# Kernel optimization log

Measured on AMD Instinct MI355X. Metric: run time of the kernel, lower is better.

## Reference

```python
import math
import jax, jax.numpy as jnp
import numpy as np

D_MODEL = 1024
N_HEAD = 16
HEAD_DIM = D_MODEL // N_HEAD
B, T = 2, 2048


def _layernorm(x, g, b, eps=1e-5):
    mu = jnp.mean(x, axis=-1, keepdims=True)
    var = jnp.mean(jnp.square(x - mu), axis=-1, keepdims=True)
    return (x - mu) * jax.lax.rsqrt(var + eps) * g + b


def _l2norm(x, eps=1e-12):
    n = jnp.sqrt(jnp.sum(jnp.square(x), axis=-1, keepdims=True))
    return x / jnp.maximum(n, eps)


def _rope(x, times):
    # x: [B,T,H,Dh] (Dh even), times: [T]
    half = x.shape[-1] // 2
    freqs = jnp.exp(-jnp.arange(half, dtype=x.dtype) * (math.log(10000.0) / half))
    theta = times[:, None] * freqs[None, :]              # [T, half]
    cos = jnp.cos(theta)[None, :, None, :]               # [1,T,1,half]
    sin = jnp.sin(theta)[None, :, None, :]
    xr = x.reshape(*x.shape[:-1], half, 2)
    x1, x2 = xr[..., 0], xr[..., 1]
    r1 = x1 * cos - x2 * sin
    r2 = x1 * sin + x2 * cos
    return jnp.stack([r1, r2], axis=-1).reshape(x.shape)


def setup_inputs() -> dict:
    key = jax.random.key(0)
    ks = jax.random.split(key, 16)
    s = 0.02
    f32 = jnp.float32
    inp = {
        'x': jax.random.normal(ks[0], (B, T, D_MODEL), f32),
        'Wq': jax.random.normal(ks[1], (D_MODEL, D_MODEL), f32) * s,
        'Wk': jax.random.normal(ks[2], (D_MODEL, D_MODEL), f32) * s,
        'Wv': jax.random.normal(ks[3], (D_MODEL, D_MODEL), f32) * s,
        'gate_w': jax.random.normal(ks[4], (D_MODEL, D_MODEL), f32) * s,
        'gate_b': jnp.zeros((D_MODEL,), f32),
        'p_w': jax.random.normal(ks[5], (D_MODEL, D_MODEL), f32) * s,
        'p_b': jnp.zeros((D_MODEL,), f32),
        'out_w': jax.random.normal(ks[6], (D_MODEL, D_MODEL), f32) * s,
        'out_b': jnp.zeros((D_MODEL,), f32),
        'clock_w': jax.random.normal(ks[7], (D_MODEL, N_HEAD), f32) * s,
        'clock_b': jnp.zeros((N_HEAD,), f32),
        'ln1_g': jnp.ones((D_MODEL,), f32), 'ln1_b': jnp.zeros((D_MODEL,), f32),
        'ln2_g': jnp.ones((D_MODEL,), f32), 'ln2_b': jnp.zeros((D_MODEL,), f32),
        'mlp_w1': jax.random.normal(ks[8], (D_MODEL, 4 * D_MODEL), f32) * s,
        'mlp_b1': jnp.zeros((4 * D_MODEL,), f32),
        'mlp_w2': jax.random.normal(ks[9], (4 * D_MODEL, D_MODEL), f32) * s,
        'mlp_b2': jnp.zeros((D_MODEL,), f32),
    }
    return inp


def reference(x, Wq, Wk, Wv, gate_w, gate_b, p_w, p_b, out_w, out_b,
              clock_w, clock_b, ln1_g, ln1_b, ln2_g, ln2_b,
              mlp_w1, mlp_b1, mlp_w2, mlp_b2):
    Bx, Tx, D = x.shape
    H, Dh = N_HEAD, HEAD_DIM
    residual = x
    xn = _layernorm(x, ln1_g, ln1_b)
    times = jnp.arange(Tx, dtype=x.dtype)

    q = _l2norm((xn @ Wq).reshape(Bx, Tx, H, Dh))
    k = _l2norm((xn @ Wk).reshape(Bx, Tx, H, Dh))
    v = (xn @ Wv).reshape(Bx, Tx, H, Dh)
    clock = jax.nn.softplus(xn @ clock_w + clock_b).reshape(Bx, Tx, H, 1)

    q = _rope(q, times)
    k = _rope(k, times)

    gj = -jax.nn.softplus(xn @ gate_w + gate_b).reshape(Bx, Tx, H, Dh)
    gcp = jnp.exp(jnp.clip(jnp.cumsum(gj, axis=1), -60.0, 50.0))
    q = q * gcp
    k = k / (gcp + 1e-8)

    p = (xn @ p_w + p_b).reshape(Bx, Tx, H, Dh)
    p_max = jnp.max(p, axis=1, keepdims=True)
    p_exp = jnp.exp(p - p_max) * clock
    p_cs = jnp.cumsum(p_exp, axis=1)
    q = q / (p_cs + 1e-8)
    k = k * p_exp

    # causal softmax attention (SDPA, scale = 1/sqrt(Dh))
    scores = jnp.einsum('bqhd,bkhd->bhqk', q, k) / math.sqrt(Dh)
    mask = jnp.tril(jnp.ones((Tx, Tx), dtype=bool))
    scores = jnp.where(mask[None, None], scores, -jnp.inf)
    attn = jax.nn.softmax(scores, axis=-1)
    out = jnp.einsum('bhqk,bkhd->bqhd', attn, v).reshape(Bx, Tx, D)

    out = out @ out_w + out_b
    x1 = out + residual
    h = _layernorm(x1, ln2_g, ln2_b)
    h = jax.nn.gelu(h @ mlp_w1 + mlp_b1, approximate=False) @ mlp_w2 + mlp_b2
    return x1 + h
```

## Files before the change

kernel.cpp:

```cpp
#include <hip/hip_runtime.h>
#include <hip/hip_bf16.h>
#include <math.h>

typedef __hip_bfloat16 bf16;
typedef __attribute__((ext_vector_type(8))) short short8;
typedef __attribute__((ext_vector_type(4))) short short4v;
typedef __attribute__((ext_vector_type(4))) float f32x4;

#define BT   4096
#define DM   1024
#define NH   16
#define DH   64
#define TSEQ 2048

__device__ __forceinline__ float wave_sum(float v){
#pragma unroll
  for (int o = 32; o; o >>= 1) v += __shfl_xor(v, o);
  return v;
}

__device__ __forceinline__ float block_sum(float v){
  __shared__ float sm[4];
  v = wave_sum(v);
  __syncthreads();
  if ((threadIdx.x & 63) == 0) sm[threadIdx.x >> 6] = v;
  __syncthreads();
  return sm[0] + sm[1] + sm[2] + sm[3];
}

__device__ __forceinline__ float softplusf(float x){
  return x > 20.f ? x : __logf(1.f + __expf(x));
}

__device__ __forceinline__ short f2bf(float f){
  unsigned u = __builtin_bit_cast(unsigned, f);
  u += 0x7FFF + ((u >> 16) & 1);
  return (short)(u >> 16);
}

__device__ __forceinline__ short8 ld8(const short* p){
  short4v a = *(const short4v*)p;
  short4v b = *(const short4v*)(p + 4);
  short8 r;
  r[0]=a[0]; r[1]=a[1]; r[2]=a[2]; r[3]=a[3];
  r[4]=b[0]; r[5]=b[1]; r[6]=b[2]; r[7]=b[3];
  return r;
}

__device__ __forceinline__ void async16(const short* g, short* l){
  __builtin_amdgcn_global_load_lds(
      (const __attribute__((address_space(1))) void*)g,
      (__attribute__((address_space(3))) void*)l, 16, 0, 0);
}

__device__ __forceinline__ int xcd_swizzle(int lin, int nwg){
  const int q = nwg >> 3, r = nwg & 7;
  const int xcd = lin & 7, i = lin >> 3;
  return (xcd < r ? xcd * (q + 1) : r * (q + 1) + (xcd - r) * q) + i;
}

__device__ __forceinline__ void wt_body(const float* __restrict__ src,
    short* __restrict__ dst, int K, int N){
  __shared__ short T[32][33];
  const int tx = threadIdx.x & 31, ty = threadIdx.x >> 5;
  const int n0 = blockIdx.x << 5, k0 = blockIdx.y << 5;
#pragma unroll
  for (int r = 0; r < 4; r++){
    const int k = k0 + (ty << 2) + r;
    const int n = n0 + tx;
    T[tx][(ty << 2) + r] = (n < N) ? f2bf(src[(long)k * N + n]) : (short)0;
  }
  __syncthreads();
#pragma unroll
  for (int r = 0; r < 4; r++){
    const int n = n0 + (ty << 2) + r;
    if (n < N) dst[(long)n * K + k0 + tx] = T[(ty << 2) + r][tx];
  }
}

__global__ __launch_bounds__(256) void wt_kernel(const float* __restrict__ src,
    short* __restrict__ dst, int K, int N){
  wt_body(src, dst, K, N);
}

__global__ __launch_bounds__(256) void wt6_kernel(
    const float* s0, const float* s1, const float* s2, const float* s3,
    const float* s4, const float* s5,
    short* d0, short* d1, short* d2, short* d3, short* d4, short* d5){
  const float* src; short* dst;
  switch (blockIdx.z){
    case 0: src = s0; dst = d0; break;
    case 1: src = s1; dst = d1; break;
    case 2: src = s2; dst = d2; break;
    case 3: src = s3; dst = d3; break;
    case 4: src = s4; dst = d4; break;
    default: src = s5; dst = d5; break;
  }
  wt_body(src, dst, DM, DM);
}

__global__ __launch_bounds__(256) void biascat_fill(const float* __restrict__ gb,
    const float* __restrict__ pb, const float* __restrict__ cb, float* __restrict__ out){
  const int i = blockIdx.x * 256 + threadIdx.x;
  if (i >= 5136) return;
  float v = 0.f;
  if (i >= 5120) v = cb[i - 5120];
  else if (i >= 4096) v = pb[i - 4096];
  else if (i >= 3072) v = gb[i - 3072];
  out[i] = v;
}

__global__ __launch_bounds__(256) void ln_kernel(const float* __restrict__ xin,
    const float* __restrict__ g, const float* __restrict__ bb, short* __restrict__ out){
  const long row = blockIdx.x;
  const int tid = threadIdx.x;
  float v[4];
#pragma unroll
  for (int i = 0; i < 4; i++) v[i] = xin[row * DM + tid + i * 256];
  float s = block_sum(v[0] + v[1] + v[2] + v[3]);
  const float mu = s * (1.f / DM);
  float d2 = 0.f;
#pragma unroll
  for (int i = 0; i < 4; i++){ float dd = v[i] - mu; d2 = fmaf(dd, dd, d2); }
  d2 = block_sum(d2);
  const float rstd = rsqrtf(d2 * (1.f / DM) + 1e-5f);
#pragma unroll
  for (int i = 0; i < 4; i++){
    int c = tid + i * 256;
    out[row * DM + c] = f2bf(fmaf((v[i] - mu) * rstd, g[c], bb[c]));
  }
}

template <int EPI>
__global__ __launch_bounds__(256) void gemm_bt(
    const short* __restrict__ A, const short* __restrict__ Bt,
    const float* __restrict__ bias, const float* __restrict__ resf,
    const float* __restrict__ bias2, float* __restrict__ Cf2,
    float* __restrict__ Cf, short* __restrict__ Cbf, int M, int N, int K)
{
  __shared__ __attribute__((aligned(16))) short As[3][4096];
  __shared__ __attribute__((aligned(16))) short Bs[3][4096];
  const int tid = threadIdx.x;
  const int lane = tid & 63, w = tid >> 6;
  const int l16 = lane & 15, quad = lane >> 4;
  const int wm = w >> 1, wn = w & 1;
  const int gx = (int)gridDim.x, gy = (int)gridDim.y;
  int wg = xcd_swizzle((int)blockIdx.x + gx * ((int)blockIdx.y + gy * (int)blockIdx.z),
                       gx * gy * (int)gridDim.z);
  const int bx = wg % gx; wg /= gx;
  const int by = wg % gy; wg /= gy;
  const int bz = wg;
  const int bm0 = by << 7, bn0 = bx << 7;
  const int ks = K / (int)gridDim.z;
  const int kbeg = bz * ks;
  const int nt = ks >> 5;

  const int csw = (tid >> 3) & 3;
  const int r0 = tid >> 2,        c0 = (tid & 3) ^ csw;
  const int r1 = 64 + (tid >> 2);
  const short* ga0 = A  + (long)(bm0 + r0) * K + kbeg + c0 * 8;
  const short* ga1 = A  + (long)(bm0 + r1) * K + kbeg + c0 * 8;
  const short* gb0 = Bt + (long)min(bn0 + r0, N - 1) * K + kbeg + c0 * 8;
  const short* gb1 = Bt + (long)min(bn0 + r1, N - 1) * K + kbeg + c0 * 8;
  const int wofs = w << 9;

#define STAGE(buf, t) do {                                   \
    const long ko_ = (long)(t) * 32;                         \
    async16(ga0 + ko_, &As[buf][wofs]);                      \
    async16(gb0 + ko_, &Bs[buf][wofs]);                      \
    async16(ga1 + ko_, &As[buf][2048 + wofs]);               \
    async16(gb1 + ko_, &Bs[buf][2048 + wofs]);               \
  } while (0)

  f32x4 acc[4][4] = {};

  STAGE(0, 0);
  if (nt > 1) STAGE(1, 1);

  const int qsw = (quad ^ ((l16 >> 1) & 3)) * 8;

  int cur = 0, stg = 2;
  for (int t = 0; t < nt; t++){
    if (t + 1 < nt){
      asm volatile("s_waitcnt vmcnt(4)" ::: "memory");
    } else {
      asm volatile("s_waitcnt vmcnt(0)" ::: "memory");
    }
    __builtin_amdgcn_s_barrier();
    __builtin_amdgcn_sched_barrier(0);
    if (t + 2 < nt) STAGE(stg, t + 2);
    short8 af[4], bfr[4];
#pragma unroll
    for (int i = 0; i < 4; i++){
      af[i]  = *(const short8*)&As[cur][(wm * 64 + i * 16 + l16) * 32 + qsw];
      bfr[i] = *(const short8*)&Bs[cur][(wn * 64 + i * 16 + l16) * 32 + qsw];
    }
#pragma unroll
    for (int i = 0; i < 4; i++)
#pragma unroll
      for (int j = 0; j < 4; j++)
        acc[i][j] = __builtin_amdgcn_mfma_f32_16x16x32_bf16(af[i], bfr[j], acc[i][j], 0, 0, 0);
    cur = (cur == 2) ? 0 : cur + 1;
    stg = (stg == 2) ? 0 : stg + 1;
  }
#undef STAGE

#pragma unroll
  for (int i = 0; i < 4; i++){
#pragma unroll
    for (int r = 0; r < 4; r++){
      const int row = bm0 + wm * 64 + i * 16 + quad * 4 + r;
#pragma unroll
      for (int j = 0; j < 4; j++){
        const int col = bn0 + wn * 64 + j * 16 + l16;
        if (col < N){
          float v = acc[i][j][r];
          const long off = (long)row * N + col;
          if constexpr (EPI >= 1 && EPI != 6) v += bias[col];
          if constexpr (EPI == 2 || EPI == 4) v += resf[off];
          if constexpr (EPI == 3){
            v = 0.5f * v * (1.f + erff(v * 0.70710678118654752f));
            Cbf[off] = f2bf(v);
          } else if constexpr (EPI == 4){
            Cf[off] = v;
            Cf2[off] = v + bias2[col];
          } else if constexpr (EPI == 6){
            unsafeAtomicAdd(&Cf[off], v);
          } else {
            Cf[off] = v;
          }
        }
      }
    }
  }
}

template <int EPI>
__global__ __launch_bounds__(256, 2) void gemm_bt2(
    const short* __restrict__ A, const short* __restrict__ Bt,
    const float* __restrict__ bias, const float* __restrict__ resf,
    float* __restrict__ Cf, short* __restrict__ Cbf, int M, int N, int K)
{
  __shared__ __attribute__((aligned(16))) short As[3][8192];
  __shared__ __attribute__((aligned(16))) short Bs[3][4096];
  const int tid = threadIdx.x;
  const int lane = tid & 63, w = tid >> 6;
  const int l16 = lane & 15, quad = lane >> 4;
  const int wm = w >> 1, wn = w & 1;
  const int gx = (int)gridDim.x, gy = (int)gridDim.y;
  int wg = xcd_swizzle((int)blockIdx.x + gx * ((int)blockIdx.y + gy * (int)blockIdx.z),
                       gx * gy * (int)gridDim.z);
  const int bx = wg % gx; wg /= gx;
  const int by = wg % gy; wg /= gy;
  const int bz = wg;
  const int bm0 = by << 8, bn0 = bx << 7;
  const int ks = K / (int)gridDim.z;
  const int kbeg = bz * ks;
  const int nt = ks >> 5;

  const int csw = (tid >> 3) & 3;
  const int c0 = (tid & 3) ^ csw;
  const int ra = tid >> 2;
  const short* ga0 = A  + (long)(bm0 + ra)       * K + kbeg + c0 * 8;
  const short* ga1 = A  + (long)(bm0 + 64 + ra)  * K + kbeg + c0 * 8;
  const short* ga2 = A  + (long)(bm0 + 128 + ra) * K + kbeg + c0 * 8;
  const short* ga3 = A  + (long)(bm0 + 192 + ra) * K + kbeg + c0 * 8;
  const short* gb0 = Bt + (long)min(bn0 + ra, N - 1)      * K + kbeg + c0 * 8;
  const short* gb1 = Bt + (long)min(bn0 + 64 + ra, N - 1) * K + kbeg + c0 * 8;
  const int wofs = w << 9;

#define STAGE2(buf, t) do {                                  \
    const long ko_ = (long)(t) * 32;                         \
    async16(ga0 + ko_, &As[buf][wofs]);                      \
    async16(ga1 + ko_, &As[buf][2048 + wofs]);               \
    async16(ga2 + ko_, &As[buf][4096 + wofs]);               \
    async16(ga3 + ko_, &As[buf][6144 + wofs]);               \
    async16(gb0 + ko_, &Bs[buf][wofs]);                      \
    async16(gb1 + ko_, &Bs[buf][2048 + wofs]);               \
  } while (0)

  f32x4 acc[8][4] = {};

  STAGE2(0, 0);
  if (nt > 1) STAGE2(1, 1);

  const int qsw = (quad ^ ((l16 >> 1) & 3)) * 8;

  int cur = 0, stg = 2;
  for (int t = 0; t < nt; t++){
    if (t + 1 < nt){
      asm volatile("s_waitcnt vmcnt(6)" ::: "memory");
    } else {
      asm volatile("s_waitcnt vmcnt(0)" ::: "memory");
    }
    __builtin_amdgcn_s_barrier();
    __builtin_amdgcn_sched_barrier(0);
    if (t + 2 < nt) STAGE2(stg, t + 2);
    short8 af[8], bfr[4];
#pragma unroll
    for (int i = 0; i < 8; i++)
      af[i]  = *(const short8*)&As[cur][(wm * 128 + i * 16 + l16) * 32 + qsw];
#pragma unroll
    for (int j = 0; j < 4; j++)
      bfr[j] = *(const short8*)&Bs[cur][(wn * 64 + j * 16 + l16) * 32 + qsw];
#pragma unroll
    for (int i = 0; i < 8; i++)
#pragma unroll
      for (int j = 0; j < 4; j++)
        acc[i][j] = __builtin_amdgcn_mfma_f32_16x16x32_bf16(af[i], bfr[j], acc[i][j], 0, 0, 0);
    cur = (cur == 2) ? 0 : cur + 1;
    stg = (stg == 2) ? 0 : stg + 1;
  }
#undef STAGE2

#pragma unroll
  for (int i = 0; i < 8; i++){
#pragma unroll
    for (int r = 0; r < 4; r++){
      const int row = bm0 + wm * 128 + i * 16 + quad * 4 + r;
#pragma unroll
      for (int j = 0; j < 4; j++){
        const int col = bn0 + wn * 64 + j * 16 + l16;
        if (col < N){
          float v = acc[i][j][r];
          const long off = (long)row * N + col;
          if constexpr (EPI >= 1 && EPI != 6) v += bias[col];
          if constexpr (EPI == 2) v += resf[off];
          if constexpr (EPI == 3){
            v = 0.5f * v * (1.f + erff(v * 0.70710678118654752f));
            Cbf[off] = f2bf(v);
          } else if constexpr (EPI == 5){
            if (col < 5120)
              Cf[(long)(col >> 10) * 4194304 + (long)row * 1024 + (col & 1023)] = v;
            else
              Cf[20971520 + (long)row * 16 + (col - 5120)] = v;
          } else if constexpr (EPI == 6){
            unsafeAtomicAdd(&Cf[off], v);
          } else {
            Cf[off] = v;
          }
        }
      }
    }
  }
}

__global__ __launch_bounds__(256) void scan_p1(float* __restrict__ G, const float* __restrict__ P,
    const float* __restrict__ Vf, short* __restrict__ Vh,
    float* __restrict__ cmax, float* __restrict__ gsum){
  const int tid = blockIdx.x * 256 + threadIdx.x;
  const int d = tid & 63, c = (tid >> 6) & 31, bh = tid >> 11;
  const int h = bh & 15, b = bh >> 4;
  const long base = (((long)(b * TSEQ + c * 64)) * NH + h) * 64 + d;
  float mx = -1e30f, gs = 0.f;
  for (int tt = 0; tt < 64; tt++){
    const long idx = base + (long)tt * (NH * 64);
    float gj = -softplusf(G[idx]);
    G[idx] = gj;
    gs += gj;
    mx = fmaxf(mx, P[idx]);
    Vh[idx] = f2bf(Vf[idx]);
  }
  const int chain = bh * 64 + d;
  cmax[chain * 32 + c] = mx;
  gsum[chain * 32 + c] = gs;
}

__global__ void scan_p2(const float* __restrict__ cmax, const float* __restrict__ gsum,
                        float* __restrict__ pmax, float* __restrict__ gpre){
  const int chain = blockIdx.x * 256 + threadIdx.x;
  float mx = -1e30f;
  for (int c = 0; c < 32; c++) mx = fmaxf(mx, cmax[chain * 32 + c]);
  pmax[chain] = mx;
  float run = 0.f;
  for (int c = 0; c < 32; c++){ gpre[chain * 32 + c] = run; run += gsum[chain * 32 + c]; }
}

__global__ __launch_bounds__(256) void scan_p3(const float* __restrict__ G, float* __restrict__ P,
    const float* __restrict__ CLKr, float* __restrict__ Q, float* __restrict__ K,
    const float* __restrict__ pmax, const float* __restrict__ gpre, float* __restrict__ psum){
  const int tid = blockIdx.x * 256 + threadIdx.x;
  const int d = tid & 63, c = (tid >> 6) & 31, bh = tid >> 11;
  const int h = bh & 15, b = bh >> 4;
  const int chain = bh * 64 + d;
  const long base = (((long)(b * TSEQ + c * 64)) * NH + h) * 64 + d;
  const float pm = pmax[chain];
  const float freq = expf(-(float)(d >> 1) * 0.28782313662425575f);
  float sn = sinf((float)(c * 64) * freq);
  float cn = cosf((float)(c * 64) * freq);
  const float sf = sinf(freq), cf = cosf(freq);
  float grun = gpre[chain * 32 + c];
  float ps = 0.f;
  for (int tt = 0; tt < 64; tt++){
    const long idx = base + (long)tt * (NH * 64);
    const int t = c * 64 + tt;
    float clk = softplusf(CLKr[(long)(b * TSEQ + t) * NH + h]);
    float pe = __expf(P[idx] - pm) * clk;
    P[idx] = pe; ps += pe;
    grun += G[idx];
    float gc = __expf(fminf(fmaxf(grun, -60.f), 50.f));
    {
      float q = Q[idx];
      float n = sqrtf(wave_sum(q * q));
      q = q / fmaxf(n, 1e-12f);
      float pr = __shfl_xor(q, 1);
      q = (d & 1) ? fmaf(pr, sn, q * cn) : fmaf(q, cn, -pr * sn);
      Q[idx] = q * gc;
    }
    {
      float k = K[idx];
      float n = sqrtf(wave_sum(k * k));
      k = k / fmaxf(n, 1e-12f);
      float pr = __shfl_xor(k, 1);
      k = (d & 1) ? fmaf(pr, sn, k * cn) : fmaf(k, cn, -pr * sn);
      K[idx] = k / (gc + 1e-8f);
    }
    const float ns = fmaf(sn, cf, cn * sf);
    const float nc = fmaf(cn, cf, -sn * sf);
    sn = ns; cn = nc;
  }
  psum[chain * 32 + c] = ps;
}

__global__ void scan_p4(const float* __restrict__ psum, float* __restrict__ ppre){
  const int chain = blockIdx.x * 256 + threadIdx.x;
  float run = 0.f;
  for (int c = 0; c < 32; c++){ ppre[chain * 32 + c] = run; run += psum[chain * 32 + c]; }
}

__global__ __launch_bounds__(256) void scan_p5(const float* __restrict__ P, const float* __restrict__ Q,
    const float* __restrict__ K, const float* __restrict__ ppre,
    short* __restrict__ Qh, short* __restrict__ Kh){
  const int tid = blockIdx.x * 256 + threadIdx.x;
  const int d = tid & 63, c = (tid >> 6) & 31, bh = tid >> 11;
  const int h = bh & 15, b = bh >> 4;
  const int chain = bh * 64 + d;
  const long base = (((long)(b * TSEQ + c * 64)) * NH + h) * 64 + d;
  float cs = ppre[chain * 32 + c];
  for (int tt = 0; tt < 64; tt++){
    const long idx = base + (long)tt * (NH * 64);
    float pe = P[idx];
    cs += pe;
    Qh[idx] = f2bf(Q[idx] / (cs + 1e-8f) * 0.125f);
    Kh[idx] = f2bf(K[idx] * pe);
  }
}

__global__ __launch_bounds__(256) void fattn_kernel(const short* __restrict__ Qh,
    const short* __restrict__ Kh, const short* __restrict__ Vh, short* __restrict__ O){
  __shared__ __attribute__((aligned(16))) short Ks[64][72];
  __shared__ __attribute__((aligned(16))) short Vt[64][68];
  __shared__ __attribute__((aligned(16))) short Ps[4][16][72];
  const int tid  = threadIdx.x;
  const int lane = tid & 63, w = tid >> 6;
  const int quad = lane >> 4, l16 = lane & 15;
  const int gx = (int)gridDim.x;
  int wgs = xcd_swizzle((int)blockIdx.x + gx * (int)blockIdx.y, gx * (int)gridDim.y);
  const int bxs = wgs % gx;
  const int bh = wgs / gx, h = bh & 15, b = bh >> 4;
  const int qt = gx - 1 - bxs;
  const int q0  = qt << 6;
  const int qw0 = q0 + w * 16;
  const long strideT = NH * DH;
  const long base_bh = ((long)b * TSEQ * NH + h) * DH;

  const short* qp = Qh + base_bh + (long)(qw0 + l16) * strideT + quad * 8;
  const short8 qa0 = *(const short8*)qp;
  const short8 qa1 = *(const short8*)(qp + 32);

  f32x4 oacc[4] = {{0,0,0,0},{0,0,0,0},{0,0,0,0},{0,0,0,0}};
  float lpart[4] = {0.f,0.f,0.f,0.f};

  const int krow = tid >> 2, kcol = (tid & 3) << 4;
  const int vkey = tid & 63, vd0 = (tid >> 6) << 4;
  const short* kbase = Kh + base_bh + (long)krow * strideT + kcol;
  const short* vbase = Vh + base_bh + (long)vkey * strideT + vd0;

  short8 kr0 = *(const short8*)kbase;
  short8 kr1 = *(const short8*)(kbase + 8);
  short8 vr0 = *(const short8*)vbase;
  short8 vr1 = *(const short8*)(vbase + 8);

  const int ntiles = qt + 1;
  for (int t = 0; t < ntiles; t++){
    *(short8*)&Ks[krow][kcol]     = kr0;
    *(short8*)&Ks[krow][kcol + 8] = kr1;
#pragma unroll
    for (int j = 0; j < 8; j++) Vt[vd0 + j][vkey] = vr0[j];
#pragma unroll
    for (int j = 0; j < 8; j++) Vt[vd0 + 8 + j][vkey] = vr1[j];
    __syncthreads();
    if (t + 1 < ntiles){
      const long off = (long)(t + 1) * (64 * strideT);
      kr0 = *(const short8*)(kbase + off);
      kr1 = *(const short8*)(kbase + off + 8);
      vr0 = *(const short8*)(vbase + off);
      vr1 = *(const short8*)(vbase + off + 8);
    }
    const int kt0 = t << 6;
    f32x4 c[4] = {{0,0,0,0},{0,0,0,0},{0,0,0,0},{0,0,0,0}};
#pragma unroll
    for (int kg = 0; kg < 4; kg++){
      const short8 b0 = ld8(&Ks[kg * 16 + l16][quad * 8]);
      const short8 b1 = ld8(&Ks[kg * 16 + l16][32 + quad * 8]);
      c[kg] = __builtin_amdgcn_mfma_f32_16x16x32_bf16(qa0, b0, c[kg], 0, 0, 0);
      c[kg] = __builtin_amdgcn_mfma_f32_16x16x32_bf16(qa1, b1, c[kg], 0, 0, 0);
    }
    if (kt0 + 63 > qw0){
#pragma unroll
      for (int kg = 0; kg < 4; kg++)
#pragma unroll
        for (int r = 0; r < 4; r++){
          const int qq = qw0 + quad * 4 + r;
          if (kt0 + kg * 16 + l16 > qq) c[kg][r] = -1e30f;
        }
    }
#pragma unroll
    for (int kg = 0; kg < 4; kg++)
#pragma unroll
      for (int r = 0; r < 4; r++) c[kg][r] = __expf(c[kg][r] - 0.25f);
#pragma unroll
    for (int r = 0; r < 4; r++)
      lpart[r] += (c[0][r] + c[1][r]) + (c[2][r] + c[3][r]);
#pragma unroll
    for (int kg = 0; kg < 4; kg++)
#pragma unroll
      for (int r = 0; r < 4; r++)
        Ps[w][quad * 4 + r][kg * 16 + l16] = f2bf(c[kg][r]);
    const short8 pa0 = ld8(&Ps[w][l16][quad * 8]);
    const short8 pa1 = ld8(&Ps[w][l16][32 + quad * 8]);
#pragma unroll
    for (int f = 0; f < 4; f++){
      const short8 vb0 = ld8(&Vt[f * 16 + l16][quad * 8]);
      const short8 vb1 = ld8(&Vt[f * 16 + l16][32 + quad * 8]);
      oacc[f] = __builtin_amdgcn_mfma_f32_16x16x32_bf16(pa0, vb0, oacc[f], 0, 0, 0);
      oacc[f] = __builtin_amdgcn_mfma_f32_16x16x32_bf16(pa1, vb1, oacc[f], 0, 0, 0);
    }
    __syncthreads();
  }
#pragma unroll
  for (int r = 0; r < 4; r++){
    float l = lpart[r];
#pragma unroll
    for (int o = 1; o <= 8; o <<= 1) l += __shfl_xor(l, o);
    const float inv = 1.f / l;
    const long row = base_bh + (long)(qw0 + quad * 4 + r) * strideT + l16;
#pragma unroll
    for (int f = 0; f < 4; f++) O[row + f * 16] = f2bf(oacc[f][r] * inv);
  }
}

extern "C" void kernel_launch(void* const* d_in, const int* in_sizes, int n_in,
                              void* d_out, int out_size, void* d_ws, size_t ws_size,
                              hipStream_t stream){
  const float* x       = (const float*)d_in[0];
  const float* Wq      = (const float*)d_in[1];
  const float* Wk      = (const float*)d_in[2];
  const float* Wv      = (const float*)d_in[3];
  const float* gate_w  = (const float*)d_in[4];
  const float* gate_b  = (const float*)d_in[5];
  const float* p_w     = (const float*)d_in[6];
  const float* p_b     = (const float*)d_in[7];
  const float* out_w   = (const float*)d_in[8];
  const float* out_b   = (const float*)d_in[9];
  const float* clock_w = (const float*)d_in[10];
  const float* clock_b = (const float*)d_in[11];
  const float* ln1_g   = (const float*)d_in[12];
  const float* ln1_b   = (const float*)d_in[13];
  const float* ln2_g   = (const float*)d_in[14];
  const float* ln2_b   = (const float*)d_in[15];
  const float* mlp_w1  = (const float*)d_in[16];
  const float* mlp_b1  = (const float*)d_in[17];
  const float* mlp_w2  = (const float*)d_in[18];
  const float* mlp_b2  = (const float*)d_in[19];
  float* outp = (float*)d_out;

  float* ws   = (float*)d_ws;
  float* C5   = ws;
  float* Qb   = ws;
  float* Kb   = ws + 4194304;
  float* Vf   = ws + 8388608;
  float* Gb   = ws + 12582912;
  float* Pb   = ws + 16777216;
  float* CLKr = ws + 20971520;
  float* cmax = CLKr + 65536;
  float* gsum = cmax + 65536;
  float* gpre = gsum + 65536;
  float* pmax = gpre + 65536;
  float* biascat = cmax;
  short* sb   = (short*)(ws + 21235712);
  short* XNb  = sb;
  short* Vh   = sb;
  short* WcT  = sb + 4194304;
  short* OwT  = WcT + 5260288;
  short* W1T  = OwT + 1048576;
  short* W2T  = W1T + 4194304;
  short* Qh  = (short*)(ws + 8388608);
  short* Kh  = (short*)(ws + 8388608 + 2097152);
  short* MID = (short*)ws;
  short* Ob  = (short*)(ws + 12582912);
  short* Hb  = (short*)(ws + 12582912 + 2097152);
  float* X1  = Pb;

  wt6_kernel<<<dim3(32, 32, 6), 256, 0, stream>>>(
      Wq, Wk, Wv, gate_w, p_w, out_w,
      WcT, WcT + 1048576, WcT + 2097152, WcT + 3145728, WcT + 4194304, OwT);
  wt_kernel<<<dim3(1, 32), 256, 0, stream>>>(clock_w, WcT + 5242880, DM, NH);
  wt_kernel<<<dim3(128, 32), 256, 0, stream>>>(mlp_w1, W1T, DM, 4 * DM);
  wt_kernel<<<dim3(32, 128), 256, 0, stream>>>(mlp_w2, W2T, 4 * DM, DM);
  biascat_fill<<<21, 256, 0, stream>>>(gate_b, p_b, clock_b, biascat);

  ln_kernel<<<BT, 256, 0, stream>>>(x, ln1_g, ln1_b, XNb);

  gemm_bt2<5><<<dim3(41, BT / 256), 256, 0, stream>>>(
      XNb, WcT, biascat, nullptr, C5, nullptr, BT, 5136, DM);

  scan_p1<<<256, 256, 0, stream>>>(Gb, Pb, Vf, Vh, cmax, gsum);
  scan_p2<<<8, 256, 0, stream>>>(cmax, gsum, pmax, gpre);
  scan_p3<<<256, 256, 0, stream>>>(Gb, Pb, CLKr, Qb, Kb, pmax, gpre, gsum);
  scan_p4<<<8, 256, 0, stream>>>(gsum, gpre);
  scan_p5<<<256, 256, 0, stream>>>(Pb, Qb, Kb, gpre, Qh, Kh);

  fattn_kernel<<<dim3(TSEQ / 64, 2 * NH), 256, 0, stream>>>(Qh, Kh, Vh, Ob);

  gemm_bt<4><<<dim3(DM / 128, BT / 128), 256, 0, stream>>>(
      Ob, OwT, out_b, x, mlp_b2, outp, X1, nullptr, BT, DM, DM);
  ln_kernel<<<BT, 256, 0, stream>>>(X1, ln2_g, ln2_b, Hb);
  gemm_bt2<3><<<dim3(4 * DM / 128, BT / 256), 256, 0, stream>>>(
      Hb, W1T, mlp_b1, nullptr, nullptr, MID, BT, 4 * DM, DM);
  gemm_bt2<6><<<dim3(DM / 128, BT / 256, 4), 256, 0, stream>>>(
      MID, W2T, nullptr, nullptr, outp, nullptr, BT, DM, 4 * DM);
}
```

Measured before the change: 644.1 us.

## Enlarge GEMM tiles to 256x256 with 512 threads and K=64 double buffering

Replaces the 256x128 triple-buffered GEMM (256 threads, K-step 32) with a 256x256 tile version using 8 waves, a K-step of 64, double buffering and an 8-way XOR swizzle. It also raises wave priority around the MFMA blocks. The aim is more operand reuse per LDS load and fewer barriers per FLOP for the big projection and MLP GEMMs. In exchange the grid has fewer blocks (for example 21x16 for the fused projection and 64 for the split-K down-projection), which risks occupancy and tail effects, and it uses 128KB of LDS per block.

```diff
diff --git a/kernel.cpp b/kernel.cpp
--- a/kernel.cpp
+++ b/kernel.cpp
@@ -236,82 +236,86 @@
 }
 
 template <int EPI>
-__global__ __launch_bounds__(256, 2) void gemm_bt2(
+__global__ __launch_bounds__(512, 2) void gemm_bt3(
     const short* __restrict__ A, const short* __restrict__ Bt,
-    const float* __restrict__ bias, const float* __restrict__ resf,
+    const float* __restrict__ bias,
     float* __restrict__ Cf, short* __restrict__ Cbf, int M, int N, int K)
 {
-  __shared__ __attribute__((aligned(16))) short As[3][8192];
-  __shared__ __attribute__((aligned(16))) short Bs[3][4096];
+  __shared__ __attribute__((aligned(16))) short As[2][16384];
+  __shared__ __attribute__((aligned(16))) short Bs[2][16384];
   const int tid = threadIdx.x;
   const int lane = tid & 63, w = tid >> 6;
   const int l16 = lane & 15, quad = lane >> 4;
-  const int wm = w >> 1, wn = w & 1;
+  const int wm = w >> 2, wn = w & 3;
   const int gx = (int)gridDim.x, gy = (int)gridDim.y;
   int wg = xcd_swizzle((int)blockIdx.x + gx * ((int)blockIdx.y + gy * (int)blockIdx.z),
                        gx * gy * (int)gridDim.z);
   const int bx = wg % gx; wg /= gx;
   const int by = wg % gy; wg /= gy;
   const int bz = wg;
-  const int bm0 = by << 8, bn0 = bx << 7;
+  const int bm0 = by << 8, bn0 = bx << 8;
   const int ks = K / (int)gridDim.z;
   const int kbeg = bz * ks;
-  const int nt = ks >> 5;
-
-  const int csw = (tid >> 3) & 3;
-  const int c0 = (tid & 3) ^ csw;
-  const int ra = tid >> 2;
-  const short* ga0 = A  + (long)(bm0 + ra)       * K + kbeg + c0 * 8;
-  const short* ga1 = A  + (long)(bm0 + 64 + ra)  * K + kbeg + c0 * 8;
-  const short* ga2 = A  + (long)(bm0 + 128 + ra) * K + kbeg + c0 * 8;
-  const short* ga3 = A  + (long)(bm0 + 192 + ra) * K + kbeg + c0 * 8;
-  const short* gb0 = Bt + (long)min(bn0 + ra, N - 1)      * K + kbeg + c0 * 8;
-  const short* gb1 = Bt + (long)min(bn0 + 64 + ra, N - 1) * K + kbeg + c0 * 8;
+  const int nt = ks >> 6;
+
+  const int rr = tid >> 3;
+  const int csw = (tid & 7) ^ (rr & 7);
+  const short* ga0 = A  + (long)(bm0 + rr)       * K + kbeg + csw * 8;
+  const short* ga1 = A  + (long)(bm0 + 64 + rr)  * K + kbeg + csw * 8;
+  const short* ga2 = A  + (long)(bm0 + 128 + rr) * K + kbeg + csw * 8;
+  const short* ga3 = A  + (long)(bm0 + 192 + rr) * K + kbeg + csw * 8;
+  const short* gb0 = Bt + (long)min(bn0 + rr, N - 1)       * K + kbeg + csw * 8;
+  const short* gb1 = Bt + (long)min(bn0 + 64 + rr, N - 1)  * K + kbeg + csw * 8;
+  const short* gb2 = Bt + (long)min(bn0 + 128 + rr, N - 1) * K + kbeg + csw * 8;
+  const short* gb3 = Bt + (long)min(bn0 + 192 + rr, N - 1) * K + kbeg + csw * 8;
   const int wofs = w << 9;
 
-#define STAGE2(buf, t) do {                                  \
-    const long ko_ = (long)(t) * 32;                         \
+#define STAGE3(buf, t) do {                                  \
+    const long ko_ = (long)(t) * 64;                         \
     async16(ga0 + ko_, &As[buf][wofs]);                      \
-    async16(ga1 + ko_, &As[buf][2048 + wofs]);               \
-    async16(ga2 + ko_, &As[buf][4096 + wofs]);               \
-    async16(ga3 + ko_, &As[buf][6144 + wofs]);               \
+    async16(ga1 + ko_, &As[buf][4096 + wofs]);               \
+    async16(ga2 + ko_, &As[buf][8192 + wofs]);               \
+    async16(ga3 + ko_, &As[buf][12288 + wofs]);              \
     async16(gb0 + ko_, &Bs[buf][wofs]);                      \
-    async16(gb1 + ko_, &Bs[buf][2048 + wofs]);               \
+    async16(gb1 + ko_, &Bs[buf][4096 + wofs]);               \
+    async16(gb2 + ko_, &Bs[buf][8192 + wofs]);               \
+    async16(gb3 + ko_, &Bs[buf][12288 + wofs]);              \
   } while (0)
 
   f32x4 acc[8][4] = {};
 
-  STAGE2(0, 0);
-  if (nt > 1) STAGE2(1, 1);
-
-  const int qsw = (quad ^ ((l16 >> 1) & 3)) * 8;
-
-  int cur = 0, stg = 2;
+  STAGE3(0, 0);
+  asm volatile("s_waitcnt vmcnt(0)" ::: "memory");
+  __builtin_amdgcn_s_barrier();
+  __builtin_amdgcn_sched_barrier(0);
+
+  int cur = 0;
   for (int t = 0; t < nt; t++){
-    if (t + 1 < nt){
-      asm volatile("s_waitcnt vmcnt(6)" ::: "memory");
-    } else {
-      asm volatile("s_waitcnt vmcnt(0)" ::: "memory");
-    }
+    if (t + 1 < nt) STAGE3(cur ^ 1, t + 1);
+#pragma unroll
+    for (int kh = 0; kh < 2; kh++){
+      const int ksw = (((kh << 2) + quad) ^ (l16 & 7)) * 8;
+      short8 af[8], bfr[4];
+#pragma unroll
+      for (int i = 0; i < 8; i++)
+        af[i] = *(const short8*)&As[cur][(wm * 128 + i * 16 + l16) * 64 + ksw];
+#pragma unroll
+      for (int j = 0; j < 4; j++)
+        bfr[j] = *(const short8*)&Bs[cur][(wn * 64 + j * 16 + l16) * 64 + ksw];
+      __builtin_amdgcn_s_setprio(1);
+#pragma unroll
+      for (int i = 0; i < 8; i++)
+#pragma unroll
+        for (int j = 0; j < 4; j++)
+          acc[i][j] = __builtin_amdgcn_mfma_f32_16x16x32_bf16(af[i], bfr[j], acc[i][j], 0, 0, 0);
+      __builtin_amdgcn_s_setprio(0);
+    }
+    asm volatile("s_waitcnt vmcnt(0)" ::: "memory");
     __builtin_amdgcn_s_barrier();
     __builtin_amdgcn_sched_barrier(0);
-    if (t + 2 < nt) STAGE2(stg, t + 2);
-    short8 af[8], bfr[4];
-#pragma unroll
-    for (int i = 0; i < 8; i++)
-      af[i]  = *(const short8*)&As[cur][(wm * 128 + i * 16 + l16) * 32 + qsw];
-#pragma unroll
-    for (int j = 0; j < 4; j++)
-      bfr[j] = *(const short8*)&Bs[cur][(wn * 64 + j * 16 + l16) * 32 + qsw];
-#pragma unroll
-    for (int i = 0; i < 8; i++)
-#pragma unroll
-      for (int j = 0; j < 4; j++)
-        acc[i][j] = __builtin_amdgcn_mfma_f32_16x16x32_bf16(af[i], bfr[j], acc[i][j], 0, 0, 0);
-    cur = (cur == 2) ? 0 : cur + 1;
-    stg = (stg == 2) ? 0 : stg + 1;
-  }
-#undef STAGE2
+    cur ^= 1;
+  }
+#undef STAGE3
 
 #pragma unroll
   for (int i = 0; i < 8; i++){
@@ -325,7 +329,6 @@
           float v = acc[i][j][r];
           const long off = (long)row * N + col;
           if constexpr (EPI >= 1 && EPI != 6) v += bias[col];
-          if constexpr (EPI == 2) v += resf[off];
           if constexpr (EPI == 3){
             v = 0.5f * v * (1.f + erff(v * 0.70710678118654752f));
             Cbf[off] = f2bf(v);
@@ -612,8 +615,8 @@
 
   ln_kernel<<<BT, 256, 0, stream>>>(x, ln1_g, ln1_b, XNb);
 
-  gemm_bt2<5><<<dim3(41, BT / 256), 256, 0, stream>>>(
-      XNb, WcT, biascat, nullptr, C5, nullptr, BT, 5136, DM);
+  gemm_bt3<5><<<dim3(21, BT / 256), 512, 0, stream>>>(
+      XNb, WcT, biascat, C5, nullptr, BT, 5136, DM);
 
   scan_p1<<<256, 256, 0, stream>>>(Gb, Pb, Vf, Vh, cmax, gsum);
   scan_p2<<<8, 256, 0, stream>>>(cmax, gsum, pmax, gpre);
@@ -626,8 +629,8 @@
   gemm_bt<4><<<dim3(DM / 128, BT / 128), 256, 0, stream>>>(
       Ob, OwT, out_b, x, mlp_b2, outp, X1, nullptr, BT, DM, DM);
   ln_kernel<<<BT, 256, 0, stream>>>(X1, ln2_g, ln2_b, Hb);
-  gemm_bt2<3><<<dim3(4 * DM / 128, BT / 256), 256, 0, stream>>>(
-      Hb, W1T, mlp_b1, nullptr, nullptr, MID, BT, 4 * DM, DM);
-  gemm_bt2<6><<<dim3(DM / 128, BT / 256, 4), 256, 0, stream>>>(
-      MID, W2T, nullptr, nullptr, outp, nullptr, BT, DM, 4 * DM);
-}
+  gemm_bt3<3><<<dim3(4 * DM / 256, BT / 256), 512, 0, stream>>>(
+      Hb, W1T, mlp_b1, nullptr, MID, BT, 4 * DM, DM);
+  gemm_bt3<6><<<dim3(DM / 256, BT / 256, 4), 512, 0, stream>>>(
+      MID, W2T, nullptr, outp, nullptr, BT, DM, 4 * DM);
+}
```

Measured after the change: 643.4 us. No clear change (-0.1%).
